# Kernel optimization log

Measured on AMD Instinct MI355X. Metric: run time of the kernel, lower is better.

Reference implementation:

```python
import jax, jax.numpy as jnp
import numpy as np
from functools import partial

NUM_QUERIES = 900
TOPK_PRE = 100      # topk(100) in source
TOPK_POST = 20      # keep_inds[:20] in source
IOU_THR = 0.7


def cxcywh_to_xyxy(b):
    cx, cy, w, h = b[..., 0], b[..., 1], b[..., 2], b[..., 3]
    return jnp.stack([cx - 0.5 * w, cy - 0.5 * h, cx + 0.5 * w, cy + 0.5 * h], axis=-1)


def nms_single(boxes, scores):
    # boxes: [K,4] xyxy, already sorted by descending score (top_k output).
    # Single class per patch in this module, so batched_nms == plain nms.
    K = boxes.shape[0]
    area = jnp.clip(boxes[:, 2] - boxes[:, 0], 0) * jnp.clip(boxes[:, 3] - boxes[:, 1], 0)
    lt = jnp.maximum(boxes[:, None, :2], boxes[None, :, :2])
    rb = jnp.minimum(boxes[:, None, 2:], boxes[None, :, 2:])
    wh = jnp.clip(rb - lt, 0)
    inter = wh[..., 0] * wh[..., 1]
    iou = inter / (area[:, None] + area[None, :] - inter + 1e-7)  # [K,K]
    idx = jnp.arange(K)

    def body(i, keep):
        sup = (iou[i] > IOU_THR) & (idx > i) & keep[i]
        return keep & (~sup)

    keep = jax.lax.fori_loop(0, K, body, jnp.ones((K,), bool))
    rank = jnp.cumsum(keep) - 1
    valid = keep & (rank < TOPK_POST)
    slot = jnp.where(valid, rank, TOPK_POST)  # invalid entries scatter into dropped slot
    sel_s = jnp.zeros((TOPK_POST + 1,), scores.dtype).at[slot].set(jnp.where(valid, scores, 0.0))[:TOPK_POST]
    sel_b = jnp.zeros((TOPK_POST + 1, 4), boxes.dtype).at[slot].set(jnp.where(valid[:, None], boxes, 0.0))[:TOPK_POST]
    vmask = jnp.zeros((TOPK_POST + 1,), bool).at[slot].set(valid)[:TOPK_POST]
    return sel_s, sel_b, vmask


def setup_inputs() -> dict:
    key = jax.random.key(0)
    k1, k2, k3, k4 = jax.random.split(key, 4)
    BS, P, Q, C = 16, 64, NUM_QUERIES, 2
    pred_logits = jax.random.normal(k1, (BS, 1, P * Q, C), jnp.float32)
    pred_boxes = jax.random.uniform(k2, (BS, 1, P * Q, 4), jnp.float32, minval=0.05, maxval=0.6)
    target_sizes = jax.random.uniform(k3, (BS, 2), jnp.float32, minval=480.0, maxval=1333.0)  # (h, w)
    labels = jax.random.randint(k4, (BS, P), 0, 80, jnp.int32)
    return {"pred_logits": pred_logits, "pred_boxes": pred_boxes,
            "target_sizes": target_sizes, "labels": labels}


def reference(pred_logits, pred_boxes, target_sizes, labels):
    BS = pred_logits.shape[0]
    Q = NUM_QUERIES
    score = jax.nn.sigmoid(pred_logits[:, 0, :, -1])          # [BS, N]
    boxes = cxcywh_to_xyxy(pred_boxes[:, 0])                   # [BS, N, 4]
    img_h, img_w = target_sizes[:, 0], target_sizes[:, 1]
    scale = jnp.stack([img_w, img_h, img_w, img_h], axis=-1)   # [BS, 4]
    boxes = boxes * scale[:, None, :]
    P = score.shape[1] // Q
    score = score.reshape(BS, P, Q)
    boxes = boxes.reshape(BS, P, Q, 4)
    top_s, top_i = jax.lax.top_k(score, TOPK_PRE)              # [BS, P, 100]
    top_b = jnp.take_along_axis(boxes, top_i[..., None], axis=2)  # [BS, P, 100, 4]
    sel_s, sel_b, vmask = jax.vmap(nms_single)(
        top_b.reshape(BS * P, TOPK_PRE, 4), top_s.reshape(BS * P, TOPK_PRE))
    sel_s = sel_s.reshape(BS, P, TOPK_POST)
    sel_b = sel_b.reshape(BS, P, TOPK_POST, 4)
    vmask = vmask.reshape(BS, P, TOPK_POST)
    sel_l = jnp.where(vmask, labels[:, :, None], -1)
    return sel_s, sel_b, sel_l, vmask
```

## Files before the change

kernel.cpp:

```cpp
#include <hip/hip_runtime.h>
#include <stdint.h>

#define NQ 900
#define TOPK_PRE 100
#define TOPK_POST 20
#define IOU_THR 0.7f
#define THREADS 512

typedef unsigned long long u64;

__device__ __forceinline__ u64 umin64(u64 a, u64 b) { return a < b ? a : b; }
__device__ __forceinline__ u64 umax64(u64 a, u64 b) { return a > b ? a : b; }

__device__ __forceinline__ void ce(u64& v, int j, bool up, int lane) {
    u64 part = __shfl_xor(v, j);
    bool lower = ((lane & j) == 0);
    v = (up == lower) ? umin64(v, part) : umax64(v, part);
}

__device__ __forceinline__ void merge_lds(const u64* __restrict__ A,
                                          const u64* __restrict__ B,
                                          u64& c0, u64& c1, int lane) {
    c0 = umin64(A[lane],      B[127 - lane]);
    c1 = umin64(A[64 + lane], B[63 - lane]);
    u64 lo = umin64(c0, c1), hi = umax64(c0, c1);
    c0 = lo; c1 = hi;
#pragma unroll
    for (int j = 32; j > 0; j >>= 1) {
        bool lower = (lane & j) == 0;
        u64 p0 = __shfl_xor(c0, j);
        u64 p1 = __shfl_xor(c1, j);
        c0 = lower ? umin64(c0, p0) : umax64(c0, p0);
        c1 = lower ? umin64(c1, p1) : umax64(c1, p1);
    }
}


__global__ __launch_bounds__(THREADS)
void ovnms_kernel(const float* __restrict__ logits,
                  const float* __restrict__ boxes,
                  const float* __restrict__ tsize,
                  const int*   __restrict__ labels,
                  float* __restrict__ out)
{
#pragma clang fp contract(off)
    const int row  = blockIdx.x;
    const int b    = row >> 6;
    const int p    = row & 63;
    const int tid  = threadIdx.x;
    const int lane = tid & 63;
    const int wid  = tid >> 6;

    __shared__ u64 wl[8 * 128];
    __shared__ u64 md[4 * 128];
    __shared__ u64 m2[2 * 128];
    __shared__ u64 fin[128];
    __shared__ float4 bslab[NQ];
    __shared__ float x1s[TOPK_PRE], y1s[TOPK_PRE], x2s[TOPK_PRE], y2s[TOPK_PRE];
    __shared__ float areas[TOPK_PRE], scs[TOPK_PRE];
    __shared__ u64 sup0[TOPK_PRE], sup1[TOPK_PRE];
    __shared__ u64 keep0s, keep1s;

    const size_t brow0 = (size_t)b * 57600 + (size_t)p * NQ;

    {
        const float4* bsrc = (const float4*)(boxes + brow0 * 4);
        if (tid < NQ) bslab[tid] = bsrc[tid];
        int t2 = tid + THREADS;
        if (t2 < NQ) bslab[t2] = bsrc[t2];
    }

    const float* lrow = logits + brow0 * 2;
    u64 c0, c1;
    {
        int q0 = wid * 128 + lane;
        int q1 = q0 + 64;
        u64 k0 = ~0ull, k1 = ~0ull;
        if (q0 < NQ) {
            float x = lrow[q0 * 2 + 1];
            float s = 1.0f / (1.0f + expf(-x));
            k0 = ((u64)(~__float_as_uint(s)) << 32) | (unsigned)q0;
        }
        if (q1 < NQ) {
            float x = lrow[q1 * 2 + 1];
            float s = 1.0f / (1.0f + expf(-x));
            k1 = ((u64)(~__float_as_uint(s)) << 32) | (unsigned)q1;
        }
        c0 = k0; c1 = k1;
    }

#pragma unroll
    for (int k = 2; k <= 64; k <<= 1) {
#pragma unroll
        for (int j = k >> 1; j > 0; j >>= 1) {
            ce(c0, j, (lane & k) == 0, lane);
            ce(c1, j, ((64 + lane) & k) == 0, lane);
        }
    }
    {
        u64 lo = umin64(c0, c1), hi = umax64(c0, c1);
        c0 = lo; c1 = hi;
#pragma unroll
        for (int j = 32; j > 0; j >>= 1) {
            ce(c0, j, true, lane);
            ce(c1, j, true, lane);
        }
    }

    wl[wid * 128 + lane]      = c0;
    wl[wid * 128 + 64 + lane] = c1;
    __syncthreads();

    if (wid < 4) {
        u64 a0, a1;
        merge_lds(&wl[(2 * wid) * 128], &wl[(2 * wid + 1) * 128], a0, a1, lane);
        md[wid * 128 + lane]      = a0;
        md[wid * 128 + 64 + lane] = a1;
    }
    __syncthreads();
    if (wid < 2) {
        u64 a0, a1;
        merge_lds(&md[(2 * wid) * 128], &md[(2 * wid + 1) * 128], a0, a1, lane);
        m2[wid * 128 + lane]      = a0;
        m2[wid * 128 + 64 + lane] = a1;
    }
    __syncthreads();
    if (wid == 0) {
        u64 a0, a1;
        merge_lds(m2, m2 + 128, a0, a1, lane);
        fin[lane]      = a0;
        fin[64 + lane] = a1;
    }
    __syncthreads();

    if (tid < TOPK_PRE) {
        u64 key = fin[tid];
        int q = (int)(key & 0xFFFFFFFFu);
        scs[tid] = __uint_as_float(~(unsigned)(key >> 32));
        float4 bx = bslab[q];
        float cx = bx.x, cy = bx.y, w = bx.z, h = bx.w;
        float ih = tsize[b * 2 + 0];
        float iw = tsize[b * 2 + 1];
        float xa = (cx - 0.5f * w) * iw;
        float ya = (cy - 0.5f * h) * ih;
        float xb = (cx + 0.5f * w) * iw;
        float yb = (cy + 0.5f * h) * ih;
        x1s[tid] = xa; y1s[tid] = ya; x2s[tid] = xb; y2s[tid] = yb;
        areas[tid] = fmaxf(xb - xa, 0.0f) * fmaxf(yb - ya, 0.0f);
    }
    __syncthreads();

    {
        const float xj1a = x1s[lane], yj1a = y1s[lane];
        const float xj2a = x2s[lane], yj2a = y2s[lane], aja = areas[lane];
        const int  j2   = lane + 64;
        const bool hv2  = j2 < TOPK_PRE;
        const int  j2c  = hv2 ? j2 : 0;
        const float xj1b = x1s[j2c], yj1b = y1s[j2c];
        const float xj2b = x2s[j2c], yj2b = y2s[j2c], ajb = areas[j2c];

#pragma unroll 4
        for (int i = wid; i < TOPK_PRE; i += 8) {
            float xi1 = x1s[i], yi1 = y1s[i], xi2 = x2s[i], yi2 = y2s[i], ai = areas[i];
            bool b0 = false;
            if (lane < i) {
                float ltx = fmaxf(xi1, xj1a);
                float lty = fmaxf(yi1, yj1a);
                float rbx = fminf(xi2, xj2a);
                float rby = fminf(yi2, yj2a);
                float wx = fmaxf(rbx - ltx, 0.0f);
                float wy = fmaxf(rby - lty, 0.0f);
                float inter = wx * wy;
                float iou = inter / (((ai + aja) - inter) + 1e-7f);
                b0 = iou > IOU_THR;
            }
            u64 m0 = __ballot(b0);
            bool b1 = false;
            if (hv2 && j2 < i) {
                float ltx = fmaxf(xi1, xj1b);
                float lty = fmaxf(yi1, yj1b);
                float rbx = fminf(xi2, xj2b);
                float rby = fminf(yi2, yj2b);
                float wx = fmaxf(rbx - ltx, 0.0f);
                float wy = fmaxf(rby - lty, 0.0f);
                float inter = wx * wy;
                float iou = inter / (((ai + ajb) - inter) + 1e-7f);
                b1 = iou > IOU_THR;
            }
            u64 m1 = __ballot(b1);
            if (lane == 0) { sup0[i] = m0; sup1[i] = m1; }
        }
    }
    __syncthreads();

    if (wid == 0) {
        u64 r0a = sup0[lane];
        u64 r1a = sup1[lane];
        const int  j2  = lane + 64;
        const bool hv2 = j2 < TOPK_PRE;
        u64 r0b = hv2 ? sup0[j2] : 0ull;
        u64 r1b = hv2 ? sup1[j2] : 0ull;
        bool alive_a = true;
        bool alive_b = hv2;

        {
            int i = 0;
            for (;;) {
                u64 act = __ballot(alive_a) & (~0ull << i);
                if (!act) break;
                i = __ffsll(act) - 1;
                alive_a = alive_a && !((r0a >> i) & 1ull);
                alive_b = alive_b && !((r0b >> i) & 1ull);
                if (++i >= 64) break;
            }
        }
        {
            int i = 0;
            for (;;) {
                u64 act = __ballot(alive_b) & (~0ull << i);
                if (!act) break;
                int m = __ffsll(act) - 1;
                if (m >= TOPK_PRE - 64) break;
                alive_a = alive_a && !((r1a >> m) & 1ull);
                alive_b = alive_b && !((r1b >> m) & 1ull);
                i = m + 1;
                if (i >= TOPK_PRE - 64) break;
            }
        }
        u64 B0 = __ballot(alive_a);
        u64 B1 = __ballot(alive_b);
        if (lane == 0) { keep0s = B0; keep1s = B1; }
    }
    __syncthreads();

    if (tid < TOPK_POST) {
        u64 K0 = keep0s, K1 = keep1s;
        int c0n = __popcll(K0);
        int idx = -1;
        if (tid < c0n) {
            u64 x = K0;
            for (int k = 0; k < tid; ++k) x &= x - 1;
            idx = __ffsll(x) - 1;
        } else {
            int t = tid - c0n;
            if (t < __popcll(K1)) {
                u64 x = K1;
                for (int k = 0; k < t; ++k) x &= x - 1;
                idx = 64 + __ffsll(x) - 1;
            }
        }
        size_t o = (size_t)row * TOPK_POST + (size_t)tid;
        float s = 0.0f, xa = 0.0f, ya = 0.0f, xb = 0.0f, yb = 0.0f;
        float lab = -1.0f, m = 0.0f;
        if (idx >= 0) {
            s = scs[idx];
            xa = x1s[idx]; ya = y1s[idx]; xb = x2s[idx]; yb = y2s[idx];
            lab = (float)labels[row];
            m = 1.0f;
        }
        out[o] = s;
        float* ob = out + 20480 + o * 4;
        ob[0] = xa; ob[1] = ya; ob[2] = xb; ob[3] = yb;
        out[102400 + o] = lab;
        out[122880 + o] = m;
    }
}

extern "C" void kernel_launch(void* const* d_in, const int* in_sizes, int n_in,
                              void* d_out, int out_size, void* d_ws, size_t ws_size,
                              hipStream_t stream) {
    const float* logits = (const float*)d_in[0];
    const float* boxes  = (const float*)d_in[1];
    const float* tsize  = (const float*)d_in[2];
    const int*   labels = (const int*)d_in[3];
    float* out = (float*)d_out;

    ovnms_kernel<<<dim3(1024), dim3(THREADS), 0, stream>>>(logits, boxes, tsize, labels, out);
}
```

Before: 38.91 us.

## Sort 32-bit score keys with rank lookup, falling back to 64-bit on ties

The bitonic sort and merge tree now run on 32-bit score-only keys instead of 64-bit score|index keys, which halves shuffle and LDS traffic. When no ties occur among the top 100, each thread binary-searches the sorted array to find its own rank and writes its box directly. This also drops the full 900-box LDS staging in favour of direct global loads for only the selected boxes. If ties are detected, a 64-bit sort fallback path runs, which adds code size and LDS usage (both key sets are declared).

```diff
diff --git a/kernel.cpp b/kernel.cpp
--- a/kernel.cpp
+++ b/kernel.cpp
@@ -8,30 +8,53 @@
 #define THREADS 512
 
 typedef unsigned long long u64;
+typedef unsigned int u32;
 
 __device__ __forceinline__ u64 umin64(u64 a, u64 b) { return a < b ? a : b; }
 __device__ __forceinline__ u64 umax64(u64 a, u64 b) { return a > b ? a : b; }
 
-__device__ __forceinline__ void ce(u64& v, int j, bool up, int lane) {
+__device__ __forceinline__ u32 ce32(u32 v, int j, bool up, int lane) {
+    u32 part = __shfl_xor(v, j);
+    bool lower = ((lane & j) == 0);
+    u32 mn = v < part ? v : part;
+    u32 mx = v < part ? part : v;
+    return (up == lower) ? mn : mx;
+}
+
+__device__ __forceinline__ void ce64(u64& v, int j, bool up, int lane) {
     u64 part = __shfl_xor(v, j);
     bool lower = ((lane & j) == 0);
     v = (up == lower) ? umin64(v, part) : umax64(v, part);
 }
 
-__device__ __forceinline__ void merge_lds(const u64* __restrict__ A,
-                                          const u64* __restrict__ B,
-                                          u64& c0, u64& c1, int lane) {
+__device__ __forceinline__ void merge_lds32(const u32* __restrict__ A,
+                                            const u32* __restrict__ B,
+                                            u32& c0, u32& c1, int lane) {
+    u32 a0 = A[lane], a1 = A[64 + lane];
+    u32 b0 = B[127 - lane], b1 = B[63 - lane];
+    c0 = a0 < b0 ? a0 : b0;
+    c1 = a1 < b1 ? a1 : b1;
+    u32 lo = c0 < c1 ? c0 : c1;
+    u32 hi = c0 < c1 ? c1 : c0;
+    c0 = lo; c1 = hi;
+#pragma unroll
+    for (int j = 32; j > 0; j >>= 1) {
+        c0 = ce32(c0, j, true, lane);
+        c1 = ce32(c1, j, true, lane);
+    }
+}
+
+__device__ __forceinline__ void merge_lds64(const u64* __restrict__ A,
+                                            const u64* __restrict__ B,
+                                            u64& c0, u64& c1, int lane) {
     c0 = umin64(A[lane],      B[127 - lane]);
     c1 = umin64(A[64 + lane], B[63 - lane]);
     u64 lo = umin64(c0, c1), hi = umax64(c0, c1);
     c0 = lo; c1 = hi;
 #pragma unroll
     for (int j = 32; j > 0; j >>= 1) {
-        bool lower = (lane & j) == 0;
-        u64 p0 = __shfl_xor(c0, j);
-        u64 p1 = __shfl_xor(c1, j);
-        c0 = lower ? umin64(c0, p0) : umax64(c0, p0);
-        c1 = lower ? umin64(c1, p1) : umax64(c1, p1);
+        ce64(c0, j, true, lane);
+        ce64(c1, j, true, lane);
     }
 }
 
@@ -51,102 +74,175 @@
     const int lane = tid & 63;
     const int wid  = tid >> 6;
 
-    __shared__ u64 wl[8 * 128];
-    __shared__ u64 md[4 * 128];
-    __shared__ u64 m2[2 * 128];
-    __shared__ u64 fin[128];
-    __shared__ float4 bslab[NQ];
+    __shared__ u32 wl32[8 * 128];
+    __shared__ u32 md32[4 * 128];
+    __shared__ u32 m232[2 * 128];
+    __shared__ u32 fin32[128];
     __shared__ float x1s[TOPK_PRE], y1s[TOPK_PRE], x2s[TOPK_PRE], y2s[TOPK_PRE];
     __shared__ float areas[TOPK_PRE], scs[TOPK_PRE];
     __shared__ u64 sup0[TOPK_PRE], sup1[TOPK_PRE];
     __shared__ u64 keep0s, keep1s;
+    __shared__ int tieflag;
+    __shared__ u64 wl64[8 * 128];
+    __shared__ u64 md64[4 * 128];
+    __shared__ u64 m264[2 * 128];
+    __shared__ u64 fin64[128];
 
     const size_t brow0 = (size_t)b * 57600 + (size_t)p * NQ;
 
+    const float* lrow = logits + brow0 * 2;
+    const int q0 = wid * 128 + lane;
+    const int q1 = q0 + 64;
+    u32 o0 = 0xFFFFFFFFu, o1 = 0xFFFFFFFFu;
+    if (q0 < NQ) {
+        float x = lrow[q0 * 2 + 1];
+        float s = 1.0f / (1.0f + expf(-x));
+        o0 = ~__float_as_uint(s);
+    }
+    if (q1 < NQ) {
+        float x = lrow[q1 * 2 + 1];
+        float s = 1.0f / (1.0f + expf(-x));
+        o1 = ~__float_as_uint(s);
+    }
+
+    u32 c0 = o0, c1 = o1;
+#pragma unroll
+    for (int k = 2; k <= 64; k <<= 1) {
+#pragma unroll
+        for (int j = k >> 1; j > 0; j >>= 1) {
+            c0 = ce32(c0, j, (lane & k) == 0, lane);
+            c1 = ce32(c1, j, ((64 + lane) & k) == 0, lane);
+        }
+    }
     {
-        const float4* bsrc = (const float4*)(boxes + brow0 * 4);
-        if (tid < NQ) bslab[tid] = bsrc[tid];
-        int t2 = tid + THREADS;
-        if (t2 < NQ) bslab[t2] = bsrc[t2];
-    }
-
-    const float* lrow = logits + brow0 * 2;
-    u64 c0, c1;
-    {
-        int q0 = wid * 128 + lane;
-        int q1 = q0 + 64;
-        u64 k0 = ~0ull, k1 = ~0ull;
-        if (q0 < NQ) {
-            float x = lrow[q0 * 2 + 1];
-            float s = 1.0f / (1.0f + expf(-x));
-            k0 = ((u64)(~__float_as_uint(s)) << 32) | (unsigned)q0;
-        }
-        if (q1 < NQ) {
-            float x = lrow[q1 * 2 + 1];
-            float s = 1.0f / (1.0f + expf(-x));
-            k1 = ((u64)(~__float_as_uint(s)) << 32) | (unsigned)q1;
-        }
-        c0 = k0; c1 = k1;
-    }
-
-#pragma unroll
-    for (int k = 2; k <= 64; k <<= 1) {
-#pragma unroll
-        for (int j = k >> 1; j > 0; j >>= 1) {
-            ce(c0, j, (lane & k) == 0, lane);
-            ce(c1, j, ((64 + lane) & k) == 0, lane);
-        }
-    }
-    {
-        u64 lo = umin64(c0, c1), hi = umax64(c0, c1);
+        u32 lo = c0 < c1 ? c0 : c1;
+        u32 hi = c0 < c1 ? c1 : c0;
         c0 = lo; c1 = hi;
 #pragma unroll
         for (int j = 32; j > 0; j >>= 1) {
-            ce(c0, j, true, lane);
-            ce(c1, j, true, lane);
-        }
-    }
-
-    wl[wid * 128 + lane]      = c0;
-    wl[wid * 128 + 64 + lane] = c1;
+            c0 = ce32(c0, j, true, lane);
+            c1 = ce32(c1, j, true, lane);
+        }
+    }
+    wl32[wid * 128 + lane]      = c0;
+    wl32[wid * 128 + 64 + lane] = c1;
     __syncthreads();
 
     if (wid < 4) {
-        u64 a0, a1;
-        merge_lds(&wl[(2 * wid) * 128], &wl[(2 * wid + 1) * 128], a0, a1, lane);
-        md[wid * 128 + lane]      = a0;
-        md[wid * 128 + 64 + lane] = a1;
+        u32 a0, a1;
+        merge_lds32(&wl32[(2 * wid) * 128], &wl32[(2 * wid + 1) * 128], a0, a1, lane);
+        md32[wid * 128 + lane]      = a0;
+        md32[wid * 128 + 64 + lane] = a1;
     }
     __syncthreads();
     if (wid < 2) {
-        u64 a0, a1;
-        merge_lds(&md[(2 * wid) * 128], &md[(2 * wid + 1) * 128], a0, a1, lane);
-        m2[wid * 128 + lane]      = a0;
-        m2[wid * 128 + 64 + lane] = a1;
-    }
+        u32 a0, a1;
+        merge_lds32(&md32[(2 * wid) * 128], &md32[(2 * wid + 1) * 128], a0, a1, lane);
+        m232[wid * 128 + lane]      = a0;
+        m232[wid * 128 + 64 + lane] = a1;
+    }
+    if (tid == 0) tieflag = 0;
     __syncthreads();
     if (wid == 0) {
-        u64 a0, a1;
-        merge_lds(m2, m2 + 128, a0, a1, lane);
-        fin[lane]      = a0;
-        fin[64 + lane] = a1;
+        u32 a0, a1;
+        merge_lds32(m232, m232 + 128, a0, a1, lane);
+        fin32[lane]      = a0;
+        fin32[64 + lane] = a1;
     }
     __syncthreads();
 
     if (tid < TOPK_PRE) {
-        u64 key = fin[tid];
-        int q = (int)(key & 0xFFFFFFFFu);
-        scs[tid] = __uint_as_float(~(unsigned)(key >> 32));
-        float4 bx = bslab[q];
-        float cx = bx.x, cy = bx.y, w = bx.z, h = bx.w;
-        float ih = tsize[b * 2 + 0];
-        float iw = tsize[b * 2 + 1];
-        float xa = (cx - 0.5f * w) * iw;
-        float ya = (cy - 0.5f * h) * ih;
-        float xb = (cx + 0.5f * w) * iw;
-        float yb = (cy + 0.5f * h) * ih;
-        x1s[tid] = xa; y1s[tid] = ya; x2s[tid] = xb; y2s[tid] = yb;
-        areas[tid] = fmaxf(xb - xa, 0.0f) * fmaxf(yb - ya, 0.0f);
+        if (fin32[tid] == fin32[tid + 1]) tieflag = 1;
+    }
+    __syncthreads();
+
+    if (!tieflag) {
+        const u32 T = fin32[TOPK_PRE - 1];
+        const float ih = tsize[b * 2 + 0];
+        const float iw = tsize[b * 2 + 1];
+#pragma unroll
+        for (int t = 0; t < 2; ++t) {
+            u32 o = t ? o1 : o0;
+            int q = t ? q1 : q0;
+            if (o <= T) {
+                int r = 0;
+#pragma unroll
+                for (int s = 64; s > 0; s >>= 1) {
+                    int m = r + s;
+                    if (m < 128 && fin32[m] <= o) r = m;
+                }
+                if (r < TOPK_PRE) {
+                    scs[r] = __uint_as_float(~o);
+                    const float* brow = boxes + (brow0 + (size_t)q) * 4;
+                    float cx = brow[0], cy = brow[1], w = brow[2], h = brow[3];
+                    float xa = (cx - 0.5f * w) * iw;
+                    float ya = (cy - 0.5f * h) * ih;
+                    float xb = (cx + 0.5f * w) * iw;
+                    float yb = (cy + 0.5f * h) * ih;
+                    x1s[r] = xa; y1s[r] = ya; x2s[r] = xb; y2s[r] = yb;
+                    areas[r] = fmaxf(xb - xa, 0.0f) * fmaxf(yb - ya, 0.0f);
+                }
+            }
+        }
+    } else {
+        u64 k0 = ((u64)o0 << 32) | (unsigned)q0;
+        u64 k1 = ((u64)o1 << 32) | (unsigned)q1;
+#pragma unroll
+        for (int k = 2; k <= 64; k <<= 1) {
+#pragma unroll
+            for (int j = k >> 1; j > 0; j >>= 1) {
+                ce64(k0, j, (lane & k) == 0, lane);
+                ce64(k1, j, ((64 + lane) & k) == 0, lane);
+            }
+        }
+        {
+            u64 lo = umin64(k0, k1), hi = umax64(k0, k1);
+            k0 = lo; k1 = hi;
+#pragma unroll
+            for (int j = 32; j > 0; j >>= 1) {
+                ce64(k0, j, true, lane);
+                ce64(k1, j, true, lane);
+            }
+        }
+        wl64[wid * 128 + lane]      = k0;
+        wl64[wid * 128 + 64 + lane] = k1;
+        __syncthreads();
+        if (wid < 4) {
+            u64 a0, a1;
+            merge_lds64(&wl64[(2 * wid) * 128], &wl64[(2 * wid + 1) * 128], a0, a1, lane);
+            md64[wid * 128 + lane]      = a0;
+            md64[wid * 128 + 64 + lane] = a1;
+        }
+        __syncthreads();
+        if (wid < 2) {
+            u64 a0, a1;
+            merge_lds64(&md64[(2 * wid) * 128], &md64[(2 * wid + 1) * 128], a0, a1, lane);
+            m264[wid * 128 + lane]      = a0;
+            m264[wid * 128 + 64 + lane] = a1;
+        }
+        __syncthreads();
+        if (wid == 0) {
+            u64 a0, a1;
+            merge_lds64(m264, m264 + 128, a0, a1, lane);
+            fin64[lane]      = a0;
+            fin64[64 + lane] = a1;
+        }
+        __syncthreads();
+        if (tid < TOPK_PRE) {
+            u64 key = fin64[tid];
+            int q = (int)(key & 0xFFFFFFFFu);
+            scs[tid] = __uint_as_float(~(unsigned)(key >> 32));
+            const float* brow = boxes + (brow0 + (size_t)q) * 4;
+            float cx = brow[0], cy = brow[1], w = brow[2], h = brow[3];
+            float ih = tsize[b * 2 + 0];
+            float iw = tsize[b * 2 + 1];
+            float xa = (cx - 0.5f * w) * iw;
+            float ya = (cy - 0.5f * h) * ih;
+            float xb = (cx + 0.5f * w) * iw;
+            float yb = (cy + 0.5f * h) * ih;
+            x1s[tid] = xa; y1s[tid] = ya; x2s[tid] = xb; y2s[tid] = yb;
+            areas[tid] = fmaxf(xb - xa, 0.0f) * fmaxf(yb - ya, 0.0f);
+        }
     }
     __syncthreads();
 
```

Result: faster. 37.91 us (-2.6%).
